# Optimization experiments

Measured on AMD Instinct MI355X. Metric: run time of the kernel, lower is better.

The kernel has to match this reference:

```python
import jax, jax.numpy as jnp
import numpy as np

H = 128  # hidden_size hard-coded in the torch module


def _lin(key, fan_in, shape):
    b = 1.0 / np.sqrt(fan_in)
    return jax.random.uniform(key, shape, minval=-b, maxval=b, dtype=jnp.float32)


def _gru_step(x, wih, bih, bhh):
    # torch GRU, single time step, h0 = 0; gate order (r, z, n)
    g = x @ wih.T + bih
    xr, xz, xn = jnp.split(g, 3, axis=-1)
    br, bz, bn = jnp.split(bhh, 3)
    r = jax.nn.sigmoid(xr + br)
    z = jax.nn.sigmoid(xz + bz)
    n = jnp.tanh(xn + r * bn)
    return (1.0 - z) * n  # h' = (1-z)*n + z*0


def _forward(x_node, x_edge, nt_w1, nt_b1, nt_w2, nt_b2, et_w, et_b,
             ngru_wih, ngru_bih, ngru_bhh, egru_wih, egru_bih, egru_bhh,
             natt_w, natt_b, eatt_w, eatt_b,
             lr_w1, lr_b1, lr_w2, lr_b2, cr_w1, cr_b1, cr_w2, cr_b2,
             mr_w1, mr_b1, mr_w2, mr_b2, pairs):
    B, N, _ = x_node.shape
    node_f = jax.nn.relu(x_node @ nt_w1 + nt_b1) @ nt_w2 + nt_b2      # [B,N,H]
    edge_f = x_edge @ et_w + et_b                                      # [B,N,N,H]
    nh = eh = None
    for _ in range(2):  # num_time_steps; GRU inputs are NOT updated in the original loop
        nh = _gru_step(node_f, ngru_wih, ngru_bih, ngru_bhh)           # [B,N,H]
        eh = _gru_step(edge_f, egru_wih, egru_bih, egru_bhh)           # [B,N,N,H]
        # --- node message pooling: attention over column index j ---
        n_col = jnp.broadcast_to(nh[:, :, None, :], eh.shape)          # aug[b,i,j] = nh[b,i]
        logits = (jnp.concatenate([n_col, eh], -1) @ natt_w)[..., 0] + natt_b[0]
        w = jax.nn.softmax(logits, axis=-1)                            # [B,N,N]
        nh = jnp.einsum('bijk,bij->bik', eh, w)                        # pooled node states
        # --- edge message pooling: 2-way attention over (row, col) node states ---
        n_row = jnp.broadcast_to(nh[:, None, :, :], eh.shape)          # [b,i,j] = nh[b,j]
        n_col = jnp.broadcast_to(nh[:, :, None, :], eh.shape)          # [b,i,j] = nh[b,i]
        l_row = (jnp.concatenate([n_row, eh], -1) @ eatt_w)[..., 0] + eatt_b[0]
        l_col = (jnp.concatenate([n_col, eh], -1) @ eatt_w)[..., 0] + eatt_b[0]
        w2 = jax.nn.softmax(jnp.stack([l_row, l_col], -1), axis=-1)    # [B,N,N,2]
        eh = w2[..., 0:1] * n_row + w2[..., 1:2] * n_col               # einsum('bijl,bijkl->bijk')
    # --- classifier inputs (aggregator = elementwise mean) ---
    i0, i1 = pairs[..., 0], pairs[..., 1]                              # [B,P]
    emb0 = jnp.take_along_axis(nh, i0[..., None], axis=1)              # [B,P,H]
    emb1 = jnp.take_along_axis(nh, i1[..., None], axis=1)
    bix = jnp.arange(B)[:, None]
    e01 = eh[bix, i0, i1]                                              # [B,P,H]
    e10 = eh[bix, i1, i0]
    ci = jnp.concatenate([(emb0 + emb1) * 0.5, (e01 + e10) * 0.5], -1)  # [B,P,2H]

    def head(w1, b1, wo, bo):
        return jax.nn.relu(ci @ w1 + b1) @ wo + bo

    lr = head(lr_w1, lr_b1, lr_w2, lr_b2)
    cr = head(cr_w1, cr_b1, cr_w2, cr_b2)
    mr = head(mr_w1, mr_b1, mr_w2, mr_b2)
    return jnp.concatenate([lr, cr, mr], axis=-1)                      # [B,P,6+5+3]


def setup_inputs() -> dict:
    B, N, P = 16, 64, 128
    NF, EF = 1024, 512
    CH = 512  # classifier hidden
    ks = list(jax.random.split(jax.random.key(0), 40))
    k = iter(ks)
    inp = {}
    inp['concatenated_node_features'] = jax.random.normal(next(k), (B, N, NF), dtype=jnp.float32)
    inp['interaction_feature'] = jax.random.normal(next(k), (B, N, N, EF), dtype=jnp.float32)
    inp['nt_w1'] = _lin(next(k), NF, (NF, 512)); inp['nt_b1'] = _lin(next(k), NF, (512,))
    inp['nt_w2'] = _lin(next(k), 512, (512, H)); inp['nt_b2'] = _lin(next(k), 512, (H,))
    inp['et_w'] = _lin(next(k), EF, (EF, H)); inp['et_b'] = _lin(next(k), EF, (H,))
    inp['ngru_wih'] = _lin(next(k), H, (3 * H, H))
    inp['ngru_bih'] = _lin(next(k), H, (3 * H,)); inp['ngru_bhh'] = _lin(next(k), H, (3 * H,))
    inp['egru_wih'] = _lin(next(k), H, (3 * H, H))
    inp['egru_bih'] = _lin(next(k), H, (3 * H,)); inp['egru_bhh'] = _lin(next(k), H, (3 * H,))
    inp['natt_w'] = _lin(next(k), 2 * H, (2 * H, 1)); inp['natt_b'] = _lin(next(k), 2 * H, (1,))
    inp['eatt_w'] = _lin(next(k), 2 * H, (2 * H, 1)); inp['eatt_b'] = _lin(next(k), 2 * H, (1,))
    for name, od in (('lr', 6), ('cr', 5), ('mr', 3)):
        inp[name + '_w1'] = _lin(next(k), 2 * H, (2 * H, CH))
        inp[name + '_b1'] = _lin(next(k), 2 * H, (CH,))
        inp[name + '_w2'] = _lin(next(k), CH, (CH, od))
        inp[name + '_b2'] = _lin(next(k), CH, (od,))
    inp['object_pairs'] = jax.random.randint(next(k), (B, P, 2), 0, N, dtype=jnp.int64 if jax.config.jax_enable_x64 else jnp.int32)
    inp['num_relation'] = jax.random.randint(next(k), (B,), 0, P, dtype=jnp.int64 if jax.config.jax_enable_x64 else jnp.int32)
    return inp


def reference(concatenated_node_features, interaction_feature,
              nt_w1, nt_b1, nt_w2, nt_b2, et_w, et_b,
              ngru_wih, ngru_bih, ngru_bhh, egru_wih, egru_bih, egru_bhh,
              natt_w, natt_b, eatt_w, eatt_b,
              lr_w1, lr_b1, lr_w2, lr_b2, cr_w1, cr_b1, cr_w2, cr_b2,
              mr_w1, mr_b1, mr_w2, mr_b2, object_pairs, num_relation):
    # num_relation is read but unused in the original make_classifier_inputs loop
    return _forward(concatenated_node_features, interaction_feature,
                    nt_w1, nt_b1, nt_w2, nt_b2, et_w, et_b,
                    ngru_wih, ngru_bih, ngru_bhh, egru_wih, egru_bih, egru_bhh,
                    natt_w, natt_b, eatt_w, eatt_b,
                    lr_w1, lr_b1, lr_w2, lr_b2, cr_w1, cr_b1, cr_w2, cr_b2,
                    mr_w1, mr_b1, mr_w2, mr_b2, object_pairs)
```

## Files before the change

### kernel.cpp

```cpp
#include <hip/hip_runtime.h>
#include <math.h>
#include <stdint.h>


typedef __attribute__((ext_vector_type(8))) short short8;
typedef __attribute__((ext_vector_type(4))) float f32x4;

#define DEVINL __device__ __forceinline__

DEVINL float sigmoidf_(float x) { return 1.0f / (1.0f + __expf(-x)); }
DEVINL float tanhf_(float x) {
    float e = __expf(2.0f * x);
    return (e - 1.0f) / (e + 1.0f);
}
DEVINL short bf16_rne(float f) {
    uint32_t u = __float_as_uint(f);
    u += 0x7FFFu + ((u >> 16) & 1u);
    return (short)(u >> 16);
}
DEVINL float bf16_to_f(short s) {
    return __uint_as_float(((uint32_t)(uint16_t)s) << 16);
}
DEVINL void cvt_hilo8(const float av[8], short8* h8, short8* l8) {
    union { uint32_t u[4]; short8 s; } H, L;
#pragma unroll
    for (int i = 0; i < 4; ++i) {
        float a0 = av[2 * i], a1 = av[2 * i + 1];
        uint32_t ph;
        asm("v_cvt_pk_bf16_f32 %0, %1, %2" : "=v"(ph) : "v"(a0), "v"(a1));
        float h0 = __uint_as_float(ph << 16);
        float h1 = __uint_as_float(ph & 0xFFFF0000u);
        uint32_t pl;
        asm("v_cvt_pk_bf16_f32 %0, %1, %2" : "=v"(pl) : "v"(a0 - h0), "v"(a1 - h1));
        H.u[i] = ph;
        L.u[i] = pl;
    }
    *h8 = H.s;
    *l8 = L.s;
}
DEVINL void gload_lds16(const void* g, void* l) {
    __builtin_amdgcn_global_load_lds(
        (const __attribute__((address_space(1))) void*)(uintptr_t)g,
        (__attribute__((address_space(3))) void*)(uint32_t)(uintptr_t)l,
        16, 0, 0);
}
DEVINL void ldsbar() {
    asm volatile("s_waitcnt lgkmcnt(0)\n\ts_barrier" ::: "memory");
    __builtin_amdgcn_sched_barrier(0);
}

__global__ __launch_bounds__(256) void prep_all(
    const float* __restrict__ et_w, const float* __restrict__ wih,
    const float* __restrict__ w1a, const float* __restrict__ w1b,
    const float* __restrict__ w1c,
    short* __restrict__ Bf1, short* __restrict__ Bf2,
    short* __restrict__ Wf1_hi, short* __restrict__ Wf1_lo)
{
    const int bid = blockIdx.x, t = threadIdx.x;
    if (bid < 256) {
        int idx = bid * 256 + t;
        int k = idx >> 7, n = idx & 127;
        float v = et_w[(size_t)k * 128 + n];
        short hi = bf16_rne(v);
        int kt = k >> 5, ct = n >> 4;
        int lane = (((k >> 3) & 3) << 4) | (n & 15);
        int j = k & 7;
        size_t s0 = (((size_t)kt * 8 + ct) * 64 + lane) * 8 + j;
        Bf1[s0] = hi;
    } else if (bid < 448) {
        int idx = (bid - 256) * 256 + t;
        int n = idx >> 7, k = idx & 127;
        float v = wih[(size_t)n * 128 + k];
        short hi = bf16_rne(v);
        int kt = k >> 5, ct = n >> 4;
        int lane = (((k >> 3) & 3) << 4) | (n & 15);
        int j = k & 7;
        size_t s0 = (((size_t)kt * 24 + ct) * 64 + lane) * 8 + j;
        Bf2[s0] = hi;
    } else {
        int idx = (bid - 448) * 256 + t;
        int h = idx >> 17;
        int r = idx & 131071;
        int k = r >> 9, c = r & 511;
        const float* w1 = (h == 0) ? w1a : (h == 1) ? w1b : w1c;
        float v = w1[(size_t)k * 512 + c];
        short hi = bf16_rne(v), lo = bf16_rne(v - bf16_to_f(hi));
        int kt = k >> 5, ct = c >> 4;
        int lane = (((k >> 3) & 3) << 4) | (c & 15);
        int j = k & 7;
        size_t fidx = ((((size_t)h * 8 + kt) * 32 + ct) * 64 + lane) * 8 + j;
        Wf1_hi[fidx] = hi;
        Wf1_lo[fidx] = lo;
    }
}

#define PH1_STEP(S, CBE0, CBE1, CBO0, CBO1, NBE0, NBE1, NBO0, NBO1,           \
                 PCV, PLD, RBUF, WBUF)                                        \
    {                                                                         \
        if ((S) < 7) {                                                        \
            const short* bke = Bf1 + (size_t)(2 * (S) + 2) * 4096;            \
            const short* bko = Bf1 + (size_t)(2 * (S) + 3) * 4096;            \
            NBE0 = *(const short8*)(bke + ct0 * 512 + ln8);                   \
            NBE1 = *(const short8*)(bke + ct1 * 512 + ln8);                   \
            NBO0 = *(const short8*)(bko + ct0 * 512 + ln8);                   \
            NBO1 = *(const short8*)(bko + ct1 * 512 + ln8);                   \
            {                                                                 \
                float av[8] = {PCV[0].x, PCV[0].y, PCV[0].z, PCV[0].w,        \
                               PCV[1].x, PCV[1].y, PCV[1].z, PCV[1].w};       \
                short8 h8, l8;                                                \
                cvt_hilo8(av, &h8, &l8);                                      \
                *(short8*)(smem + (WBUF) + aslotb) = h8;                      \
                *(short8*)(smem + (WBUF) + 4096 + aslotb) = l8;               \
            }                                                                 \
            {                                                                 \
                float av[8] = {PCV[2].x, PCV[2].y, PCV[2].z, PCV[2].w,        \
                               PCV[3].x, PCV[3].y, PCV[3].z, PCV[3].w};       \
                short8 h8, l8;                                                \
                cvt_hilo8(av, &h8, &l8);                                      \
                *(short8*)(smem + (WBUF) + 8192 + aslotb) = h8;               \
                *(short8*)(smem + (WBUF) + 12288 + aslotb) = l8;              \
            }                                                                 \
        }                                                                     \
        if ((S) < 6) {                                                        \
            PLD[0] = *(const float4*)(aptr + (size_t)(2 * (S) + 4) * 32);     \
            PLD[1] = *(const float4*)(aptr + (size_t)(2 * (S) + 4) * 32 + 4); \
            PLD[2] = *(const float4*)(aptr + (size_t)(2 * (S) + 5) * 32);     \
            PLD[3] = *(const float4*)(aptr + (size_t)(2 * (S) + 5) * 32 + 4); \
        }                                                                     \
        {                                                                     \
            const char* base = smem + (RBUF);                                 \
            short8 Ahf[4], Alf[4];                                            \
            _Pragma("unroll") for (int rt = 0; rt < 4; ++rt) {                \
                Ahf[rt] = *(const short8*)(base + (rt * 64 + lane) * 16);     \
                Alf[rt] = *(const short8*)(base + 4096 + (rt * 64 + lane) * 16); \
            }                                                                 \
            _Pragma("unroll") for (int rt = 0; rt < 4; ++rt) {                \
                acc1[rt][0] = __builtin_amdgcn_mfma_f32_16x16x32_bf16(Ahf[rt], CBE0, acc1[rt][0], 0, 0, 0); \
                acc1[rt][0] = __builtin_amdgcn_mfma_f32_16x16x32_bf16(Alf[rt], CBE0, acc1[rt][0], 0, 0, 0); \
                acc1[rt][1] = __builtin_amdgcn_mfma_f32_16x16x32_bf16(Ahf[rt], CBE1, acc1[rt][1], 0, 0, 0); \
                acc1[rt][1] = __builtin_amdgcn_mfma_f32_16x16x32_bf16(Alf[rt], CBE1, acc1[rt][1], 0, 0, 0); \
            }                                                                 \
            _Pragma("unroll") for (int rt = 0; rt < 4; ++rt) {                \
                Ahf[rt] = *(const short8*)(base + 8192 + (rt * 64 + lane) * 16); \
                Alf[rt] = *(const short8*)(base + 12288 + (rt * 64 + lane) * 16); \
            }                                                                 \
            _Pragma("unroll") for (int rt = 0; rt < 4; ++rt) {                \
                acc1[rt][0] = __builtin_amdgcn_mfma_f32_16x16x32_bf16(Ahf[rt], CBO0, acc1[rt][0], 0, 0, 0); \
                acc1[rt][0] = __builtin_amdgcn_mfma_f32_16x16x32_bf16(Alf[rt], CBO0, acc1[rt][0], 0, 0, 0); \
                acc1[rt][1] = __builtin_amdgcn_mfma_f32_16x16x32_bf16(Ahf[rt], CBO1, acc1[rt][1], 0, 0, 0); \
                acc1[rt][1] = __builtin_amdgcn_mfma_f32_16x16x32_bf16(Alf[rt], CBO1, acc1[rt][1], 0, 0, 0); \
            }                                                                 \
        }                                                                     \
        ldsbar();                                                             \
    }

__global__ __launch_bounds__(256, 3) void fused_kernel(
    const float* __restrict__ x_edge,
    const short* __restrict__ Bf1, const short* __restrict__ Bf2,
    const float* __restrict__ et_b,
    const float* __restrict__ bih, const float* __restrict__ bhh,
    const float* __restrict__ natt_w, const float* __restrict__ eatt_w,
    float* __restrict__ nh_p, float* __restrict__ u_out)
{
    __shared__ __align__(16) char smem[35328];
    const int t = threadIdx.x;
    const int wv = t >> 6, lane = t & 63;
    const int g = blockIdx.x;
    const size_t bm = (size_t)g * 64;

    const int arow = t >> 2, akb = t & 3;
    const int aslotb = (((arow >> 4) * 64) + ((akb << 4) | (arow & 15))) * 16;
    const float* aptr = x_edge + (bm + arow) * 512 + akb * 8;

    const int ct0 = wv * 2, ct1 = wv * 2 + 1;
    const int ln8 = lane * 8;

    f32x4 acc1[4][2] = {};

    float4 paX[4], paY[4];
    short8 bAe0, bAe1, bAo0, bAo1, bBe0, bBe1, bBo0, bBo1;

    {
        float4 t0 = *(const float4*)(aptr);
        float4 t1 = *(const float4*)(aptr + 4);
        float4 t2 = *(const float4*)(aptr + 32);
        float4 t3 = *(const float4*)(aptr + 36);
        paX[0] = *(const float4*)(aptr + 64);
        paX[1] = *(const float4*)(aptr + 68);
        paX[2] = *(const float4*)(aptr + 96);
        paX[3] = *(const float4*)(aptr + 100);
        bAe0 = *(const short8*)(Bf1 + ct0 * 512 + ln8);
        bAe1 = *(const short8*)(Bf1 + ct1 * 512 + ln8);
        bAo0 = *(const short8*)(Bf1 + 4096 + ct0 * 512 + ln8);
        bAo1 = *(const short8*)(Bf1 + 4096 + ct1 * 512 + ln8);
        {
            float av[8] = {t0.x, t0.y, t0.z, t0.w, t1.x, t1.y, t1.z, t1.w};
            short8 h8, l8;
            cvt_hilo8(av, &h8, &l8);
            *(short8*)(smem + aslotb) = h8;
            *(short8*)(smem + 4096 + aslotb) = l8;
        }
        {
            float av[8] = {t2.x, t2.y, t2.z, t2.w, t3.x, t3.y, t3.z, t3.w};
            short8 h8, l8;
            cvt_hilo8(av, &h8, &l8);
            *(short8*)(smem + 8192 + aslotb) = h8;
            *(short8*)(smem + 12288 + aslotb) = l8;
        }
    }
    ldsbar();

    for (int s = 0; s < 8; s += 2) {
        PH1_STEP(s,     bAe0, bAe1, bAo0, bAo1, bBe0, bBe1, bBo0, bBo1,
                 paX, paY, 0, 16384)
        PH1_STEP(s + 1, bBe0, bBe1, bBo0, bBo1, bAe0, bAe1, bAo0, bAo1,
                 paY, paX, 16384, 0)
    }
    __syncthreads();

    float* ef_s = (float*)smem;
#pragma unroll
    for (int c = 0; c < 2; ++c) {
        int col = wv * 32 + c * 16 + (lane & 15);
        float bias = et_b[col];
#pragma unroll
        for (int rt = 0; rt < 4; ++rt) {
#pragma unroll
            for (int q = 0; q < 4; ++q) {
                int row = rt * 16 + ((lane >> 4) << 2) + q;
                ef_s[row * 132 + col] = acc1[rt][c][q] + bias;
            }
        }
    }
    __syncthreads();

    const int EHP = 132;
    float* eh_s = (float*)smem;
#pragma unroll
    for (int rtp = 0; rtp < 2; ++rtp) {
        f32x4 acch[2][6] = {};
#pragma unroll
        for (int kt = 0; kt < 4; ++kt) {
            const short* bkt = Bf2 + (size_t)kt * 12288;
            short8 Ah[2], Al[2];
#pragma unroll
            for (int r = 0; r < 2; ++r) {
                int rt = rtp * 2 + r;
                const float* src = ef_s + (rt * 16 + (lane & 15)) * 132
                                 + kt * 32 + (lane >> 4) * 8;
                float4 v0 = *(const float4*)(src);
                float4 v1 = *(const float4*)(src + 4);
                float av[8] = {v0.x, v0.y, v0.z, v0.w, v1.x, v1.y, v1.z, v1.w};
                cvt_hilo8(av, &Ah[r], &Al[r]);
            }
#pragma unroll
            for (int c = 0; c < 6; ++c) {
                int ctg = ((c >> 1) << 3) + (wv << 1) + (c & 1);
                short8 Bh = *(const short8*)(bkt + ctg * 512 + ln8);
#pragma unroll
                for (int r = 0; r < 2; ++r) {
                    acch[r][c] = __builtin_amdgcn_mfma_f32_16x16x32_bf16(Ah[r], Bh, acch[r][c], 0, 0, 0);
                    acch[r][c] = __builtin_amdgcn_mfma_f32_16x16x32_bf16(Al[r], Bh, acch[r][c], 0, 0, 0);
                }
            }
        }
        __syncthreads();
#pragma unroll
        for (int cc = 0; cc < 2; ++cc) {
            int o = (wv << 5) + (cc << 4) + (lane & 15);
            float bco = bih[o] + bhh[o];
            float bcz = bih[128 + o] + bhh[128 + o];
            float bcn = bih[256 + o];
            float bn3 = bhh[256 + o];
#pragma unroll
            for (int r = 0; r < 2; ++r) {
#pragma unroll
                for (int q = 0; q < 4; ++q) {
                    int row = rtp * 32 + r * 16 + ((lane >> 4) << 2) + q;
                    float rr = sigmoidf_(acch[r][cc][q] + bco);
                    float zz = sigmoidf_(acch[r][2 + cc][q] + bcz);
                    float nn = tanhf_(acch[r][4 + cc][q] + bcn + rr * bn3);
                    eh_s[row * EHP + o] = (1.0f - zz) * nn;
                }
            }
        }
    }
    __syncthreads();

    float* red  = (float*)(smem + 33792);
    float* s2v  = red + 256;
    float* ewv  = s2v + 64;
    {
        int j = t >> 2, q = t & 3;
        const float* row = eh_s + j * EHP + q * 32;
        const float* wb = natt_w + 128 + q * 32;
        float a = 0.f;
#pragma unroll
        for (int k2 = 0; k2 < 32; ++k2) a = fmaf(row[k2], wb[k2], a);
        red[t] = a;
    }
    __syncthreads();
    if (t < 64) s2v[t] = red[4 * t] + red[4 * t + 1] + red[4 * t + 2] + red[4 * t + 3];
    __syncthreads();
    float sv = s2v[lane];
    float m = sv;
#pragma unroll
    for (int d = 32; d; d >>= 1) m = fmaxf(m, __shfl_xor(m, d, 64));
    float e = __expf(sv - m);
    float ssum = e;
#pragma unroll
    for (int d = 32; d; d >>= 1) ssum += __shfl_xor(ssum, d, 64);
    float inv = 1.0f / ssum;
    if (wv == 0) ewv[lane] = e;
    __syncthreads();
    {
        int o = t & 127, h = t >> 7;
        float a = 0.f;
        for (int j = h * 32; j < h * 32 + 32; ++j)
            a = fmaf(ewv[j], eh_s[j * EHP + o], a);
        __syncthreads();
        red[t] = a;
    }
    __syncthreads();
    if (t < 128) {
        float v = (red[t] + red[t + 128]) * inv;
        nh_p[(size_t)g * 128 + t] = v;
        red[t] = v * eatt_w[t];
    }
    __syncthreads();
    for (int s = 64; s > 0; s >>= 1) {
        if (t < s) red[t] += red[t + s];
        __syncthreads();
    }
    if (t == 0) u_out[g] = red[0];
}

__global__ __launch_bounds__(128) void ci_kernel(
    const float* __restrict__ nh_p, const float* __restrict__ u,
    const int* __restrict__ pairs, float* __restrict__ ci)
{
    const int bp = blockIdx.x;
    const int b  = bp >> 7;
    const int t  = threadIdx.x;
    int i0 = pairs[bp * 2 + 0];
    int i1 = pairs[bp * 2 + 1];
    const float* n0 = nh_p + (size_t)(b * 64 + i0) * 128;
    const float* n1 = nh_p + (size_t)(b * 64 + i1) * 128;
    float s = sigmoidf_(u[b * 64 + i1] - u[b * 64 + i0]);
    float v0 = n0[t], v1 = n1[t];
    ci[(size_t)bp * 256 + t]       = 0.5f * (v0 + v1);
    ci[(size_t)bp * 256 + 128 + t] = s * v1 + (1.0f - s) * v0;
}

__global__ __launch_bounds__(256, 1) void headcls_kernel(
    const float* __restrict__ ci,
    const short* __restrict__ Wf1_hi, const short* __restrict__ Wf1_lo,
    const float* __restrict__ b1a, const float* __restrict__ b1b,
    const float* __restrict__ b1c,
    const float* __restrict__ w2a, const float* __restrict__ w2b,
    const float* __restrict__ w2c,
    const float* __restrict__ b2a, const float* __restrict__ b2b,
    const float* __restrict__ b2c,
    float* __restrict__ out)
{
    __shared__ __align__(16) char smem[139264];
    const int t = threadIdx.x;
    const int wv = t >> 6, lane = t & 63;
    const int rb = blockIdx.x;
    const int hd = blockIdx.y;
    const float* b1 = hd == 0 ? b1a : hd == 1 ? b1b : b1c;
    const float* w2 = hd == 0 ? w2a : hd == 1 ? w2b : w2c;
    const float* b2 = hd == 0 ? b2a : hd == 1 ? b2b : b2c;
    const int od  = hd == 0 ? 6 : hd == 1 ? 5 : 3;
    const int off = hd == 0 ? 0 : hd == 1 ? 6 : 11;

    const int arow = t >> 2, akb = t & 3;
    const int abyte = ((((arow >> 4) * 64) + ((akb << 4) | (arow & 15))) * 8) * 2;
    const float* aptr = ci + ((size_t)rb * 32 + arow) * 256 + akb * 8;

    f32x4 acc[2][8] = {};

    float4 a0, a1;
    if (t < 128) {
        a0 = *(const float4*)(aptr);
        a1 = *(const float4*)(aptr + 4);
    }
    {
        const char* sh = (const char*)(Wf1_hi + (size_t)hd * 8 * 32 * 512);
        const char* sl = (const char*)(Wf1_lo + (size_t)hd * 8 * 32 * 512);
#pragma unroll
        for (int i = 0; i < 8; ++i) {
            int ch = i * 4 + wv;
            int o2 = ch * 1024 + lane * 16;
            gload_lds16(sh + o2, smem + ch * 1024);
            gload_lds16(sl + o2, smem + 32768 + ch * 1024);
        }
    }
    if (t < 128) {
        float av[8] = {a0.x, a0.y, a0.z, a0.w, a1.x, a1.y, a1.z, a1.w};
        short8 h8, l8;
        cvt_hilo8(av, &h8, &l8);
        *(short8*)(smem + 131072 + abyte) = h8;
        *(short8*)(smem + 131072 + 2048 + abyte) = l8;
    }
    __syncthreads();

    for (int kt = 0; kt < 8; ++kt) {
        const int cur = kt & 1;
        const char* Bh_c = smem + cur * 65536;
        const char* Bl_c = Bh_c + 32768;
        const char* Ah_c = smem + 131072 + cur * 4096;
        const char* Al_c = Ah_c + 2048;

        float4 b0, b1v;
        if (kt < 7) {
            const char* sh = (const char*)(Wf1_hi + ((size_t)hd * 8 + kt + 1) * 32 * 512);
            const char* sl = (const char*)(Wf1_lo + ((size_t)hd * 8 + kt + 1) * 32 * 512);
            char* dBh = smem + (cur ^ 1) * 65536;
#pragma unroll
            for (int i = 0; i < 8; ++i) {
                int ch = i * 4 + wv;
                int o2 = ch * 1024 + lane * 16;
                gload_lds16(sh + o2, dBh + ch * 1024);
                gload_lds16(sl + o2, dBh + 32768 + ch * 1024);
            }
            if (t < 128) {
                b0  = *(const float4*)(aptr + (size_t)(kt + 1) * 32);
                b1v = *(const float4*)(aptr + (size_t)(kt + 1) * 32 + 4);
            }
        }

        short8 Ah[2], Al[2];
#pragma unroll
        for (int rt = 0; rt < 2; ++rt) {
            Ah[rt] = *(const short8*)(Ah_c + (rt * 64 + lane) * 16);
            Al[rt] = *(const short8*)(Al_c + (rt * 64 + lane) * 16);
        }
#pragma unroll
        for (int c = 0; c < 8; ++c) {
            int ctg = wv * 8 + c;
            short8 Bh = *(const short8*)(Bh_c + (ctg * 64 + lane) * 16);
            short8 Bl = *(const short8*)(Bl_c + (ctg * 64 + lane) * 16);
#pragma unroll
            for (int rt = 0; rt < 2; ++rt) {
                acc[rt][c] = __builtin_amdgcn_mfma_f32_16x16x32_bf16(Ah[rt], Bh, acc[rt][c], 0, 0, 0);
                acc[rt][c] = __builtin_amdgcn_mfma_f32_16x16x32_bf16(Al[rt], Bh, acc[rt][c], 0, 0, 0);
                acc[rt][c] = __builtin_amdgcn_mfma_f32_16x16x32_bf16(Ah[rt], Bl, acc[rt][c], 0, 0, 0);
            }
        }

        if (kt < 7 && t < 128) {
            float av[8] = {b0.x, b0.y, b0.z, b0.w, b1v.x, b1v.y, b1v.z, b1v.w};
            short8 h8, l8;
            cvt_hilo8(av, &h8, &l8);
            char* dAh = smem + 131072 + (cur ^ 1) * 4096;
            *(short8*)(dAh + abyte) = h8;
            *(short8*)(dAh + 2048 + abyte) = l8;
        }
        __syncthreads();
    }

    float* h_s  = (float*)smem;
    float* w2_s = (float*)(smem + 66048);
    for (int idx = t; idx < 512 * od; idx += 256) w2_s[idx] = w2[idx];
#pragma unroll
    for (int c = 0; c < 8; ++c) {
        int ctg = wv * 8 + c;
        int col = ctg * 16 + (lane & 15);
        float bias = b1[col];
#pragma unroll
        for (int rt = 0; rt < 2; ++rt) {
#pragma unroll
            for (int q = 0; q < 4; ++q) {
                int row = rt * 16 + ((lane >> 4) << 2) + q;
                h_s[row * 516 + col] = fmaxf(acc[rt][c][q] + bias, 0.f);
            }
        }
    }
    __syncthreads();

    {
        int row = t >> 3, o = t & 7;
        if (o < od) {
            const float* hr = h_s + row * 516;
            float a = b2[o];
            for (int c = 0; c < 512; ++c)
                a = fmaf(hr[c], w2_s[c * od + o], a);
            out[((size_t)rb * 32 + row) * 14 + off + o] = a;
        }
    }
}

extern "C" void kernel_launch(void* const* d_in, const int* in_sizes, int n_in,
                              void* d_out, int out_size, void* d_ws, size_t ws_size,
                              hipStream_t stream)
{
    const float* x_edge   = (const float*)d_in[1];
    const float* et_w     = (const float*)d_in[6];
    const float* et_b     = (const float*)d_in[7];
    const float* egru_wih = (const float*)d_in[11];
    const float* egru_bih = (const float*)d_in[12];
    const float* egru_bhh = (const float*)d_in[13];
    const float* natt_w   = (const float*)d_in[14];
    const float* eatt_w   = (const float*)d_in[16];
    const float* lr_w1 = (const float*)d_in[18];
    const float* lr_b1 = (const float*)d_in[19];
    const float* lr_w2 = (const float*)d_in[20];
    const float* lr_b2 = (const float*)d_in[21];
    const float* cr_w1 = (const float*)d_in[22];
    const float* cr_b1 = (const float*)d_in[23];
    const float* cr_w2 = (const float*)d_in[24];
    const float* cr_b2 = (const float*)d_in[25];
    const float* mr_w1 = (const float*)d_in[26];
    const float* mr_b1 = (const float*)d_in[27];
    const float* mr_w2 = (const float*)d_in[28];
    const float* mr_b2 = (const float*)d_in[29];
    const int* pairs   = (const int*)d_in[30];
    float* out = (float*)d_out;
    char* ws = (char*)d_ws;

    short* Bf1    = (short*)(ws + 0);
    short* Bf2    = (short*)(ws + 131072);
    short* Wf1_hi = (short*)(ws + 229376);
    short* Wf1_lo = (short*)(ws + 1015808);
    float* nh_p   = (float*)(ws + 1802240);
    float* u      = (float*)(ws + 2326528);
    float* ci     = (float*)(ws + 2330624);

    prep_all<<<1984, 256, 0, stream>>>(et_w, egru_wih, lr_w1, cr_w1, mr_w1,
                                       Bf1, Bf2, Wf1_hi, Wf1_lo);

    fused_kernel<<<1024, 256, 0, stream>>>(
        x_edge, Bf1, Bf2, et_b, egru_bih, egru_bhh, natt_w, eatt_w, nh_p, u);

    ci_kernel<<<2048, 128, 0, stream>>>(nh_p, u, pairs, ci);

    headcls_kernel<<<dim3(64, 3), 256, 0, stream>>>(
        ci, Wf1_hi, Wf1_lo, lr_b1, cr_b1, mr_b1,
        lr_w2, cr_w2, mr_w2, lr_b2, cr_b2, mr_b2, out);
}
```

Baseline: 80.94 us.

## Process two row groups per block and prefetch next group's inputs during epilogue

The fused kernel now launches half as many blocks, and each block loops over two 64-row groups. The first x_edge and weight fragments of the second group are loaded right after the first group's phase-1 MFMA loop, so that load overlaps with the first group's GRU and attention epilogue. This targets the exposed global-load latency at the start of each block, but it halves the block count (512 blocks on a 256-CU device) and adds live registers, which may hurt occupancy and load balance.

```diff
diff --git a/kernel.cpp b/kernel.cpp
--- a/kernel.cpp
+++ b/kernel.cpp
@@ -165,174 +165,196 @@
     __shared__ __align__(16) char smem[35328];
     const int t = threadIdx.x;
     const int wv = t >> 6, lane = t & 63;
-    const int g = blockIdx.x;
-    const size_t bm = (size_t)g * 64;
 
     const int arow = t >> 2, akb = t & 3;
     const int aslotb = (((arow >> 4) * 64) + ((akb << 4) | (arow & 15))) * 16;
-    const float* aptr = x_edge + (bm + arow) * 512 + akb * 8;
-
     const int ct0 = wv * 2, ct1 = wv * 2 + 1;
     const int ln8 = lane * 8;
 
-    f32x4 acc1[4][2] = {};
-
-    float4 paX[4], paY[4];
+    float4 pa0[4], paX[4], paY[4];
     short8 bAe0, bAe1, bAo0, bAo1, bBe0, bBe1, bBo0, bBo1;
 
     {
-        float4 t0 = *(const float4*)(aptr);
-        float4 t1 = *(const float4*)(aptr + 4);
-        float4 t2 = *(const float4*)(aptr + 32);
-        float4 t3 = *(const float4*)(aptr + 36);
-        paX[0] = *(const float4*)(aptr + 64);
-        paX[1] = *(const float4*)(aptr + 68);
-        paX[2] = *(const float4*)(aptr + 96);
-        paX[3] = *(const float4*)(aptr + 100);
+        const float* ap = x_edge + ((size_t)blockIdx.x * 128 + arow) * 512 + akb * 8;
+        pa0[0] = *(const float4*)(ap);
+        pa0[1] = *(const float4*)(ap + 4);
+        pa0[2] = *(const float4*)(ap + 32);
+        pa0[3] = *(const float4*)(ap + 36);
+        paX[0] = *(const float4*)(ap + 64);
+        paX[1] = *(const float4*)(ap + 68);
+        paX[2] = *(const float4*)(ap + 96);
+        paX[3] = *(const float4*)(ap + 100);
         bAe0 = *(const short8*)(Bf1 + ct0 * 512 + ln8);
         bAe1 = *(const short8*)(Bf1 + ct1 * 512 + ln8);
         bAo0 = *(const short8*)(Bf1 + 4096 + ct0 * 512 + ln8);
         bAo1 = *(const short8*)(Bf1 + 4096 + ct1 * 512 + ln8);
+    }
+
+    for (int gi = 0; gi < 2; ++gi) {
+        const int g = blockIdx.x * 2 + gi;
+        const size_t bm = (size_t)g * 64;
+        const float* aptr = x_edge + (bm + arow) * 512 + akb * 8;
+
         {
-            float av[8] = {t0.x, t0.y, t0.z, t0.w, t1.x, t1.y, t1.z, t1.w};
+            float av[8] = {pa0[0].x, pa0[0].y, pa0[0].z, pa0[0].w,
+                           pa0[1].x, pa0[1].y, pa0[1].z, pa0[1].w};
             short8 h8, l8;
             cvt_hilo8(av, &h8, &l8);
             *(short8*)(smem + aslotb) = h8;
             *(short8*)(smem + 4096 + aslotb) = l8;
         }
         {
-            float av[8] = {t2.x, t2.y, t2.z, t2.w, t3.x, t3.y, t3.z, t3.w};
+            float av[8] = {pa0[2].x, pa0[2].y, pa0[2].z, pa0[2].w,
+                           pa0[3].x, pa0[3].y, pa0[3].z, pa0[3].w};
             short8 h8, l8;
             cvt_hilo8(av, &h8, &l8);
             *(short8*)(smem + 8192 + aslotb) = h8;
             *(short8*)(smem + 12288 + aslotb) = l8;
         }
-    }
-    ldsbar();
-
-    for (int s = 0; s < 8; s += 2) {
-        PH1_STEP(s,     bAe0, bAe1, bAo0, bAo1, bBe0, bBe1, bBo0, bBo1,
-                 paX, paY, 0, 16384)
-        PH1_STEP(s + 1, bBe0, bBe1, bBo0, bBo1, bAe0, bAe1, bAo0, bAo1,
-                 paY, paX, 16384, 0)
-    }
-    __syncthreads();
-
-    float* ef_s = (float*)smem;
-#pragma unroll
-    for (int c = 0; c < 2; ++c) {
-        int col = wv * 32 + c * 16 + (lane & 15);
-        float bias = et_b[col];
-#pragma unroll
-        for (int rt = 0; rt < 4; ++rt) {
-#pragma unroll
-            for (int q = 0; q < 4; ++q) {
-                int row = rt * 16 + ((lane >> 4) << 2) + q;
-                ef_s[row * 132 + col] = acc1[rt][c][q] + bias;
-            }
-        }
-    }
-    __syncthreads();
-
-    const int EHP = 132;
-    float* eh_s = (float*)smem;
-#pragma unroll
-    for (int rtp = 0; rtp < 2; ++rtp) {
-        f32x4 acch[2][6] = {};
-#pragma unroll
-        for (int kt = 0; kt < 4; ++kt) {
-            const short* bkt = Bf2 + (size_t)kt * 12288;
-            short8 Ah[2], Al[2];
-#pragma unroll
-            for (int r = 0; r < 2; ++r) {
-                int rt = rtp * 2 + r;
-                const float* src = ef_s + (rt * 16 + (lane & 15)) * 132
-                                 + kt * 32 + (lane >> 4) * 8;
-                float4 v0 = *(const float4*)(src);
-                float4 v1 = *(const float4*)(src + 4);
-                float av[8] = {v0.x, v0.y, v0.z, v0.w, v1.x, v1.y, v1.z, v1.w};
-                cvt_hilo8(av, &Ah[r], &Al[r]);
-            }
-#pragma unroll
-            for (int c = 0; c < 6; ++c) {
-                int ctg = ((c >> 1) << 3) + (wv << 1) + (c & 1);
-                short8 Bh = *(const short8*)(bkt + ctg * 512 + ln8);
+        ldsbar();
+
+        f32x4 acc1[4][2] = {};
+        for (int s = 0; s < 8; s += 2) {
+            PH1_STEP(s,     bAe0, bAe1, bAo0, bAo1, bBe0, bBe1, bBo0, bBo1,
+                     paX, paY, 0, 16384)
+            PH1_STEP(s + 1, bBe0, bBe1, bBo0, bBo1, bAe0, bAe1, bAo0, bAo1,
+                     paY, paX, 16384, 0)
+        }
+
+        if (gi == 0) {
+            const float* apN = x_edge + (bm + 64 + arow) * 512 + akb * 8;
+            pa0[0] = *(const float4*)(apN);
+            pa0[1] = *(const float4*)(apN + 4);
+            pa0[2] = *(const float4*)(apN + 32);
+            pa0[3] = *(const float4*)(apN + 36);
+            paX[0] = *(const float4*)(apN + 64);
+            paX[1] = *(const float4*)(apN + 68);
+            paX[2] = *(const float4*)(apN + 96);
+            paX[3] = *(const float4*)(apN + 100);
+            bAe0 = *(const short8*)(Bf1 + ct0 * 512 + ln8);
+            bAe1 = *(const short8*)(Bf1 + ct1 * 512 + ln8);
+            bAo0 = *(const short8*)(Bf1 + 4096 + ct0 * 512 + ln8);
+            bAo1 = *(const short8*)(Bf1 + 4096 + ct1 * 512 + ln8);
+        }
+        __syncthreads();
+
+        float* ef_s = (float*)smem;
+#pragma unroll
+        for (int c = 0; c < 2; ++c) {
+            int col = wv * 32 + c * 16 + (lane & 15);
+            float bias = et_b[col];
+#pragma unroll
+            for (int rt = 0; rt < 4; ++rt) {
+#pragma unroll
+                for (int q = 0; q < 4; ++q) {
+                    int row = rt * 16 + ((lane >> 4) << 2) + q;
+                    ef_s[row * 132 + col] = acc1[rt][c][q] + bias;
+                }
+            }
+        }
+        __syncthreads();
+
+        const int EHP = 132;
+        float* eh_s = (float*)smem;
+#pragma unroll
+        for (int rtp = 0; rtp < 2; ++rtp) {
+            f32x4 acch[2][6] = {};
+#pragma unroll
+            for (int kt = 0; kt < 4; ++kt) {
+                const short* bkt = Bf2 + (size_t)kt * 12288;
+                short8 Ah[2], Al[2];
 #pragma unroll
                 for (int r = 0; r < 2; ++r) {
-                    acch[r][c] = __builtin_amdgcn_mfma_f32_16x16x32_bf16(Ah[r], Bh, acch[r][c], 0, 0, 0);
-                    acch[r][c] = __builtin_amdgcn_mfma_f32_16x16x32_bf16(Al[r], Bh, acch[r][c], 0, 0, 0);
+                    int rt = rtp * 2 + r;
+                    const float* src = ef_s + (rt * 16 + (lane & 15)) * 132
+                                     + kt * 32 + (lane >> 4) * 8;
+                    float4 v0 = *(const float4*)(src);
+                    float4 v1 = *(const float4*)(src + 4);
+                    float av[8] = {v0.x, v0.y, v0.z, v0.w, v1.x, v1.y, v1.z, v1.w};
+                    cvt_hilo8(av, &Ah[r], &Al[r]);
                 }
-            }
-        }
-        __syncthreads();
-#pragma unroll
-        for (int cc = 0; cc < 2; ++cc) {
-            int o = (wv << 5) + (cc << 4) + (lane & 15);
-            float bco = bih[o] + bhh[o];
-            float bcz = bih[128 + o] + bhh[128 + o];
-            float bcn = bih[256 + o];
-            float bn3 = bhh[256 + o];
-#pragma unroll
-            for (int r = 0; r < 2; ++r) {
-#pragma unroll
-                for (int q = 0; q < 4; ++q) {
-                    int row = rtp * 32 + r * 16 + ((lane >> 4) << 2) + q;
-                    float rr = sigmoidf_(acch[r][cc][q] + bco);
-                    float zz = sigmoidf_(acch[r][2 + cc][q] + bcz);
-                    float nn = tanhf_(acch[r][4 + cc][q] + bcn + rr * bn3);
-                    eh_s[row * EHP + o] = (1.0f - zz) * nn;
+#pragma unroll
+                for (int c = 0; c < 6; ++c) {
+                    int ctg = ((c >> 1) << 3) + (wv << 1) + (c & 1);
+                    short8 Bh = *(const short8*)(bkt + ctg * 512 + ln8);
+#pragma unroll
+                    for (int r = 0; r < 2; ++r) {
+                        acch[r][c] = __builtin_amdgcn_mfma_f32_16x16x32_bf16(Ah[r], Bh, acch[r][c], 0, 0, 0);
+                        acch[r][c] = __builtin_amdgcn_mfma_f32_16x16x32_bf16(Al[r], Bh, acch[r][c], 0, 0, 0);
+                    }
                 }
             }
-        }
-    }
-    __syncthreads();
-
-    float* red  = (float*)(smem + 33792);
-    float* s2v  = red + 256;
-    float* ewv  = s2v + 64;
-    {
-        int j = t >> 2, q = t & 3;
-        const float* row = eh_s + j * EHP + q * 32;
-        const float* wb = natt_w + 128 + q * 32;
-        float a = 0.f;
-#pragma unroll
-        for (int k2 = 0; k2 < 32; ++k2) a = fmaf(row[k2], wb[k2], a);
-        red[t] = a;
-    }
-    __syncthreads();
-    if (t < 64) s2v[t] = red[4 * t] + red[4 * t + 1] + red[4 * t + 2] + red[4 * t + 3];
-    __syncthreads();
-    float sv = s2v[lane];
-    float m = sv;
-#pragma unroll
-    for (int d = 32; d; d >>= 1) m = fmaxf(m, __shfl_xor(m, d, 64));
-    float e = __expf(sv - m);
-    float ssum = e;
-#pragma unroll
-    for (int d = 32; d; d >>= 1) ssum += __shfl_xor(ssum, d, 64);
-    float inv = 1.0f / ssum;
-    if (wv == 0) ewv[lane] = e;
-    __syncthreads();
-    {
-        int o = t & 127, h = t >> 7;
-        float a = 0.f;
-        for (int j = h * 32; j < h * 32 + 32; ++j)
-            a = fmaf(ewv[j], eh_s[j * EHP + o], a);
-        __syncthreads();
-        red[t] = a;
-    }
-    __syncthreads();
-    if (t < 128) {
-        float v = (red[t] + red[t + 128]) * inv;
-        nh_p[(size_t)g * 128 + t] = v;
-        red[t] = v * eatt_w[t];
-    }
-    __syncthreads();
-    for (int s = 64; s > 0; s >>= 1) {
-        if (t < s) red[t] += red[t + s];
-        __syncthreads();
-    }
-    if (t == 0) u_out[g] = red[0];
+            __syncthreads();
+#pragma unroll
+            for (int cc = 0; cc < 2; ++cc) {
+                int o = (wv << 5) + (cc << 4) + (lane & 15);
+                float bco = bih[o] + bhh[o];
+                float bcz = bih[128 + o] + bhh[128 + o];
+                float bcn = bih[256 + o];
+                float bn3 = bhh[256 + o];
+#pragma unroll
+                for (int r = 0; r < 2; ++r) {
+#pragma unroll
+                    for (int q = 0; q < 4; ++q) {
+                        int row = rtp * 32 + r * 16 + ((lane >> 4) << 2) + q;
+                        float rr = sigmoidf_(acch[r][cc][q] + bco);
+                        float zz = sigmoidf_(acch[r][2 + cc][q] + bcz);
+                        float nn = tanhf_(acch[r][4 + cc][q] + bcn + rr * bn3);
+                        eh_s[row * EHP + o] = (1.0f - zz) * nn;
+                    }
+                }
+            }
+        }
+        __syncthreads();
+
+        float* red  = (float*)(smem + 33792);
+        float* s2v  = red + 256;
+        float* ewv  = s2v + 64;
+        {
+            int j = t >> 2, q = t & 3;
+            const float* row = eh_s + j * EHP + q * 32;
+            const float* wb = natt_w + 128 + q * 32;
+            float a = 0.f;
+#pragma unroll
+            for (int k2 = 0; k2 < 32; ++k2) a = fmaf(row[k2], wb[k2], a);
+            red[t] = a;
+        }
+        __syncthreads();
+        if (t < 64) s2v[t] = red[4 * t] + red[4 * t + 1] + red[4 * t + 2] + red[4 * t + 3];
+        __syncthreads();
+        float sv = s2v[lane];
+        float m = sv;
+#pragma unroll
+        for (int d = 32; d; d >>= 1) m = fmaxf(m, __shfl_xor(m, d, 64));
+        float e = __expf(sv - m);
+        float ssum = e;
+#pragma unroll
+        for (int d = 32; d; d >>= 1) ssum += __shfl_xor(ssum, d, 64);
+        float inv = 1.0f / ssum;
+        if (wv == 0) ewv[lane] = e;
+        __syncthreads();
+        {
+            int o = t & 127, h = t >> 7;
+            float a = 0.f;
+            for (int j = h * 32; j < h * 32 + 32; ++j)
+                a = fmaf(ewv[j], eh_s[j * EHP + o], a);
+            __syncthreads();
+            red[t] = a;
+        }
+        __syncthreads();
+        if (t < 128) {
+            float v = (red[t] + red[t + 128]) * inv;
+            nh_p[(size_t)g * 128 + t] = v;
+            red[t] = v * eatt_w[t];
+        }
+        __syncthreads();
+        for (int s = 64; s > 0; s >>= 1) {
+            if (t < s) red[t] += red[t + s];
+            __syncthreads();
+        }
+        if (t == 0) u_out[g] = red[0];
+        __syncthreads();
+    }
 }
 
 __global__ __launch_bounds__(128) void ci_kernel(
@@ -530,7 +552,7 @@
     prep_all<<<1984, 256, 0, stream>>>(et_w, egru_wih, lr_w1, cr_w1, mr_w1,
                                        Bf1, Bf2, Wf1_hi, Wf1_lo);
 
-    fused_kernel<<<1024, 256, 0, stream>>>(
+    fused_kernel<<<512, 256, 0, stream>>>(
         x_edge, Bf1, Bf2, et_b, egru_bih, egru_bhh, natt_w, eatt_w, nh_p, u);
 
     ci_kernel<<<2048, 128, 0, stream>>>(nh_p, u, pairs, ci);
```

Result: slower. 133.3 us (+64.7%).
